# Kernel tuning notes

Hardware: AMD Instinct MI355X
Metric: run time of the kernel (lower is better)

Reference implementation:

```python
import jax, jax.numpy as jnp
import numpy as np

NODES_PER_GRAPH = 128


def _leaky(x):
    return jnp.where(x >= 0, x, 0.01 * x)


def _graph_conv(x, W, src, dst, w_e, n_nodes):
    # DGL GraphConv, norm='both', bias=False, with edge_weight.
    # Structural (unweighted) degrees, clamped to 1, as in DGL.
    ones = jnp.ones(src.shape[0], dtype=x.dtype)
    deg_out = jnp.clip(jax.ops.segment_sum(ones, src, num_segments=n_nodes), 1.0)
    deg_in = jnp.clip(jax.ops.segment_sum(ones, dst, num_segments=n_nodes), 1.0)
    x = x * (deg_out ** -0.5)[:, None]
    if W.shape[0] > W.shape[1]:  # in_feats > out_feats: project first (DGL order)
        x = x @ W
    msg = x[src] * w_e[:, None]                     # [E, d]
    agg = jax.ops.segment_sum(msg, dst, num_segments=n_nodes)
    agg = agg * (deg_in ** -0.5)[:, None]
    if W.shape[0] <= W.shape[1]:
        agg = agg @ W
    return agg


def setup_inputs() -> dict:
    key = jax.random.key(0)
    ks = jax.random.split(key, 8)
    N, E = 131072, 1048576
    in_feats, hidden, readout = 64, 256, 128
    return {
        "node_feats": jax.random.normal(ks[0], (N, in_feats), dtype=jnp.float32),
        "edge_weight": jax.random.uniform(ks[1], (E,), dtype=jnp.float32),
        "W1": jax.random.normal(ks[2], (in_feats, hidden), dtype=jnp.float32) * 0.1,
        "W2": jax.random.normal(ks[3], (hidden, readout), dtype=jnp.float32) * 0.05,
        "W_lin": jax.random.normal(ks[4], (readout, 64), dtype=jnp.float32) * 0.1,
        "W_cls": jax.random.normal(ks[5], (64, 16), dtype=jnp.float32) * 0.1,
        "edge_src": jax.random.randint(ks[6], (E,), 0, N, dtype=jnp.int32),
        "edge_dst": jax.random.randint(ks[7], (E,), 0, N, dtype=jnp.int32),
    }


def reference(node_feats, edge_weight, W1, W2, W_lin, W_cls, edge_src, edge_dst):
    N = node_feats.shape[0]
    G = N // NODES_PER_GRAPH
    h = _leaky(_graph_conv(node_feats, W1, edge_src, edge_dst, edge_weight, N))
    h = _leaky(_graph_conv(h, W2, edge_src, edge_dst, edge_weight, N))
    # mean_nodes readout over batched graphs of equal size
    gid = jnp.arange(N, dtype=jnp.int32) // NODES_PER_GRAPH
    pooled = jax.ops.segment_sum(h, gid, num_segments=G) / NODES_PER_GRAPH
    # linear -> dropout(eval: identity) -> classifier (no activation in head)
    return (pooled @ W_lin) @ W_cls
```

## Files before the change

### kernel.cpp

```cpp
#include <hip/hip_runtime.h>


constexpr int NPG = 128;
constexpr int F0  = 64;
constexpr int F1  = 256;
constexpr int F2  = 128;
constexpr int BMM = 64;
constexpr int H2  = 136;
constexpr int CAP = 40;
constexpr int NXCD = 8;

using bf16x8 = __attribute__((ext_vector_type(8))) short;
using f32x4  = __attribute__((ext_vector_type(4))) float;

__device__ __forceinline__ float leaky(float x) {
    return (x >= 0.f) ? x : 0.01f * x;
}

__device__ __forceinline__ unsigned short f2bf(float x) {
    unsigned u = __float_as_uint(x);
    return (unsigned short)((u + 0x7FFFu + ((u >> 16) & 1u)) >> 16);
}
__device__ __forceinline__ float bf2f(unsigned short h) {
    return __uint_as_float(((unsigned)h) << 16);
}
__device__ __forceinline__ void split2(float x, unsigned short& hi, unsigned short& lo) {
    hi = f2bf(x);
    lo = f2bf(x - bf2f(hi));
}

__device__ __forceinline__ f32x4 mfma16(bf16x8 a, bf16x8 b, f32x4 c) {
    return __builtin_amdgcn_mfma_f32_16x16x32_bf16(a, b, c, 0, 0, 0);
}


__global__ void k_count_fill(const int* __restrict__ src, const int* __restrict__ dst,
                             const float* __restrict__ we,
                             int* __restrict__ cnt_priv,
                             int* __restrict__ cnt_dst,
                             int2* __restrict__ slots, unsigned E, int N) {
    unsigned xcc;
    asm("s_getreg_b32 %0, hwreg(HW_REG_XCC_ID)" : "=s"(xcc));
    xcc &= (NXCD - 1);
    unsigned e = blockIdx.x * 256u + threadIdx.x;
    if (e < E) {
        const int s = src[e], d = dst[e];
        const int pos = atomicAdd(&cnt_dst[d], 1);
        if (pos < CAP) slots[(size_t)d * CAP + pos] = make_int2(s, __float_as_int(we[e]));
        __hip_atomic_fetch_add(&cnt_priv[(size_t)xcc * N + s], 1,
                               __ATOMIC_RELAXED, __HIP_MEMORY_SCOPE_WORKGROUP);
    }
}

__global__ void k_finalize_deg(const int* __restrict__ cnt_priv,
                               const int* __restrict__ cnt_dst,
                               float* __restrict__ dinv_out, float* __restrict__ dinv_in,
                               int N) {
    int i = blockIdx.x * blockDim.x + threadIdx.x;
    if (i < N) {
        int c = 0;
#pragma unroll
        for (int x = 0; x < NXCD; ++x) c += cnt_priv[(size_t)x * N + i];
        dinv_out[i] = rsqrtf((float)max(c, 1));
        dinv_in[i]  = rsqrtf((float)max(cnt_dst[i], 1));
    }
}

__global__ void __launch_bounds__(256) k_scale_w(
        int2* __restrict__ slots, const int* __restrict__ cnt_dst,
        const float* __restrict__ dinv_out, int N) {
    int gid = blockIdx.x * 256 + threadIdx.x;
    int n = gid >> 3;
    int j0 = gid & 7;
    if (n >= N) return;
    const int cnt = min(cnt_dst[n], CAP);
    for (int j = j0; j < cnt; j += 8) {
        const size_t idx = (size_t)n * CAP + j;
        int2 p = slots[idx];
        p.y = __float_as_int(__int_as_float(p.y) * dinv_out[p.x]);
        slots[idx] = p;
    }
}

__global__ void k_wsplit1(const float* __restrict__ W1,
                          unsigned short* __restrict__ w1h, unsigned short* __restrict__ w1l) {
    int i = blockIdx.x * 256 + threadIdx.x;
    if (i < F1 * F0) {
        int n = i >> 6, k = i & 63;
        unsigned short h, l;
        split2(W1[k * F1 + n], h, l);
        w1h[i] = h; w1l[i] = l;
    }
}
__global__ void k_wsplit2(const float* __restrict__ W2,
                          unsigned short* __restrict__ w2h, unsigned short* __restrict__ w2l) {
    int i = blockIdx.x * 256 + threadIdx.x;
    if (i < F2 * F1) {
        int n = i >> 8, k = i & 255;
        unsigned short h, l;
        split2(W2[k * F2 + n], h, l);
        w2h[i] = h; w2l[i] = l;
    }
}

__global__ void __launch_bounds__(256) k_gather1(
        const float4* __restrict__ featsv, const int* __restrict__ cnt_dst,
        const int2* __restrict__ slots, const float* __restrict__ dinv_in,
        unsigned short* __restrict__ a1h, unsigned short* __restrict__ a1l, int N) {
    const int gid = blockIdx.x * 256 + threadIdx.x;
    const int n = gid >> 4;
    const int s = gid & 15;
    if (n >= N) return;
    const size_t b = (size_t)n * CAP;
    const int cnt = min(cnt_dst[n], CAP);
    float4 acc = make_float4(0.f, 0.f, 0.f, 0.f);
    int j = 0;
    for (; j + 4 <= cnt; j += 4) {
        const int2 p0 = slots[b + j], p1 = slots[b + j + 1];
        const int2 p2 = slots[b + j + 2], p3 = slots[b + j + 3];
        const float4 v0 = featsv[(size_t)p0.x * 16 + s];
        const float4 v1 = featsv[(size_t)p1.x * 16 + s];
        const float4 v2 = featsv[(size_t)p2.x * 16 + s];
        const float4 v3 = featsv[(size_t)p3.x * 16 + s];
        const float w0 = __int_as_float(p0.y), w1 = __int_as_float(p1.y);
        const float w2 = __int_as_float(p2.y), w3 = __int_as_float(p3.y);
        acc.x = fmaf(v0.x, w0, acc.x); acc.y = fmaf(v0.y, w0, acc.y);
        acc.z = fmaf(v0.z, w0, acc.z); acc.w = fmaf(v0.w, w0, acc.w);
        acc.x = fmaf(v1.x, w1, acc.x); acc.y = fmaf(v1.y, w1, acc.y);
        acc.z = fmaf(v1.z, w1, acc.z); acc.w = fmaf(v1.w, w1, acc.w);
        acc.x = fmaf(v2.x, w2, acc.x); acc.y = fmaf(v2.y, w2, acc.y);
        acc.z = fmaf(v2.z, w2, acc.z); acc.w = fmaf(v2.w, w2, acc.w);
        acc.x = fmaf(v3.x, w3, acc.x); acc.y = fmaf(v3.y, w3, acc.y);
        acc.z = fmaf(v3.z, w3, acc.z); acc.w = fmaf(v3.w, w3, acc.w);
    }
    for (; j < cnt; ++j) {
        const int2 p = slots[b + j];
        const float4 v = featsv[(size_t)p.x * 16 + s];
        const float w = __int_as_float(p.y);
        acc.x = fmaf(v.x, w, acc.x); acc.y = fmaf(v.y, w, acc.y);
        acc.z = fmaf(v.z, w, acc.z); acc.w = fmaf(v.w, w, acc.w);
    }
    const float din = dinv_in[n];
    ushort4 h4, l4;
    split2(acc.x * din, h4.x, l4.x);
    split2(acc.y * din, h4.y, l4.y);
    split2(acc.z * din, h4.z, l4.z);
    split2(acc.w * din, h4.w, l4.w);
    const size_t off = (size_t)n * 64 + s * 4;
    *(ushort4*)(a1h + off) = h4;
    *(ushort4*)(a1l + off) = l4;
}

__global__ void __launch_bounds__(256, 4) k_mfma_fused(
        const unsigned short* __restrict__ a1h, const unsigned short* __restrict__ a1l,
        const unsigned short* __restrict__ w1h, const unsigned short* __restrict__ w1l,
        const unsigned short* __restrict__ w2h, const unsigned short* __restrict__ w2l,
        unsigned short* __restrict__ x2b) {
    __shared__ unsigned short hhi[BMM][H2];
    __shared__ unsigned short hlo[BMM][H2];
    const int tid  = threadIdx.x;
    const int w    = tid >> 6;
    const int lane = tid & 63;
    const int r    = lane & 15;
    const int kg   = lane >> 4;
    const int base = blockIdx.x * BMM;

    f32x4 acc1[4][4] = {};
#pragma unroll
    for (int ks = 0; ks < 2; ++ks) {
        const int kk = ks * 32 + kg * 8;
        bf16x8 wh[4], wl[4];
#pragma unroll
        for (int j = 0; j < 4; ++j) {
            const int col = (j >> 1) * 128 + w * 32 + (j & 1) * 16 + r;
            wh[j] = *(const bf16x8*)(w1h + col * F0 + kk);
            wl[j] = *(const bf16x8*)(w1l + col * F0 + kk);
        }
#pragma unroll
        for (int mt = 0; mt < 4; ++mt) {
            const size_t aoff = (size_t)(base + mt * 16 + r) * F0 + kk;
            const bf16x8 ah = *(const bf16x8*)(a1h + aoff);
            const bf16x8 al = *(const bf16x8*)(a1l + aoff);
#pragma unroll
            for (int j = 0; j < 4; ++j) {
                acc1[mt][j] = mfma16(ah, wh[j], acc1[mt][j]);
                acc1[mt][j] = mfma16(ah, wl[j], acc1[mt][j]);
                acc1[mt][j] = mfma16(al, wh[j], acc1[mt][j]);
            }
        }
    }

    f32x4 acc2[4][2] = {};
    const int c2base = w * 32;
#pragma unroll
    for (int h = 0; h < 2; ++h) {
#pragma unroll
        for (int jn = 0; jn < 2; ++jn) {
            const int j = h * 2 + jn;
            const int lc = w * 32 + jn * 16 + r;
#pragma unroll
            for (int mt = 0; mt < 4; ++mt)
#pragma unroll
                for (int i = 0; i < 4; ++i) {
                    const int rl = mt * 16 + kg * 4 + i;
                    unsigned short hi_, lo_;
                    split2(leaky(acc1[mt][j][i]), hi_, lo_);
                    hhi[rl][lc] = hi_;
                    hlo[rl][lc] = lo_;
                }
        }
        __syncthreads();
#pragma unroll
        for (int ks = 0; ks < 4; ++ks) {
            const int lkk = ks * 32 + kg * 8;
            const int kglob = h * 128 + lkk;
            bf16x8 w2hv[2], w2lv[2];
#pragma unroll
            for (int nt = 0; nt < 2; ++nt) {
                const int col = c2base + nt * 16 + r;
                w2hv[nt] = *(const bf16x8*)(w2h + col * F1 + kglob);
                w2lv[nt] = *(const bf16x8*)(w2l + col * F1 + kglob);
            }
#pragma unroll
            for (int mt = 0; mt < 4; ++mt) {
                const int rl = mt * 16 + r;
                const bf16x8 ah = *(const bf16x8*)&hhi[rl][lkk];
                const bf16x8 al = *(const bf16x8*)&hlo[rl][lkk];
#pragma unroll
                for (int nt = 0; nt < 2; ++nt) {
                    acc2[mt][nt] = mfma16(ah, w2hv[nt], acc2[mt][nt]);
                    acc2[mt][nt] = mfma16(ah, w2lv[nt], acc2[mt][nt]);
                    acc2[mt][nt] = mfma16(al, w2hv[nt], acc2[mt][nt]);
                }
            }
        }
        __syncthreads();
    }

#pragma unroll
    for (int mt = 0; mt < 4; ++mt)
#pragma unroll
        for (int nt = 0; nt < 2; ++nt)
#pragma unroll
            for (int i = 0; i < 4; ++i) {
                const int row = base + mt * 16 + kg * 4 + i;
                const int col = c2base + nt * 16 + r;
                x2b[(size_t)row * F2 + col] = f2bf(acc2[mt][nt][i]);
            }
}

__global__ void __launch_bounds__(256) k_gather2_pool4(
        const ushort4* __restrict__ x2v, const int* __restrict__ cnt_dst,
        const int2* __restrict__ slots, const float* __restrict__ dinv_in,
        float* __restrict__ pooled) {
    const int g = blockIdx.x >> 2;
    const int c = blockIdx.x & 3;
    const int t = threadIdx.x;
    const int q = t >> 3;
    const int s = t & 7;
    const int d4 = c * 8 + s;

    float4 pool = make_float4(0.f, 0.f, 0.f, 0.f);
    const int nbase = g * NPG;
#pragma unroll
    for (int i = 0; i < NPG; i += 32) {
        const int n = nbase + i + q;
        const size_t b = (size_t)n * CAP;
        const int cnt = min(cnt_dst[n], CAP);
        float4 acc = make_float4(0.f, 0.f, 0.f, 0.f);
        int j = 0;
        for (; j + 4 <= cnt; j += 4) {
            const int2 p0 = slots[b + j], p1 = slots[b + j + 1];
            const int2 p2 = slots[b + j + 2], p3 = slots[b + j + 3];
            const ushort4 u0 = x2v[(size_t)p0.x * 32 + d4];
            const ushort4 u1 = x2v[(size_t)p1.x * 32 + d4];
            const ushort4 u2 = x2v[(size_t)p2.x * 32 + d4];
            const ushort4 u3 = x2v[(size_t)p3.x * 32 + d4];
            const float w0 = __int_as_float(p0.y), w1 = __int_as_float(p1.y);
            const float w2 = __int_as_float(p2.y), w3 = __int_as_float(p3.y);
            acc.x = fmaf(bf2f(u0.x), w0, acc.x); acc.y = fmaf(bf2f(u0.y), w0, acc.y);
            acc.z = fmaf(bf2f(u0.z), w0, acc.z); acc.w = fmaf(bf2f(u0.w), w0, acc.w);
            acc.x = fmaf(bf2f(u1.x), w1, acc.x); acc.y = fmaf(bf2f(u1.y), w1, acc.y);
            acc.z = fmaf(bf2f(u1.z), w1, acc.z); acc.w = fmaf(bf2f(u1.w), w1, acc.w);
            acc.x = fmaf(bf2f(u2.x), w2, acc.x); acc.y = fmaf(bf2f(u2.y), w2, acc.y);
            acc.z = fmaf(bf2f(u2.z), w2, acc.z); acc.w = fmaf(bf2f(u2.w), w2, acc.w);
            acc.x = fmaf(bf2f(u3.x), w3, acc.x); acc.y = fmaf(bf2f(u3.y), w3, acc.y);
            acc.z = fmaf(bf2f(u3.z), w3, acc.z); acc.w = fmaf(bf2f(u3.w), w3, acc.w);
        }
        for (; j < cnt; ++j) {
            const int2 p = slots[b + j];
            const float w = __int_as_float(p.y);
            const ushort4 u = x2v[(size_t)p.x * 32 + d4];
            acc.x = fmaf(bf2f(u.x), w, acc.x); acc.y = fmaf(bf2f(u.y), w, acc.y);
            acc.z = fmaf(bf2f(u.z), w, acc.z); acc.w = fmaf(bf2f(u.w), w, acc.w);
        }
        const float din = dinv_in[n];
        pool.x += leaky(acc.x * din);
        pool.y += leaky(acc.y * din);
        pool.z += leaky(acc.z * din);
        pool.w += leaky(acc.w * din);
    }

    __shared__ float4 pl[32][8];
    pl[q][s] = pool;
    __syncthreads();
#pragma unroll
    for (int off = 16; off >= 1; off >>= 1) {
        if (q < off) {
            const float4 o = pl[q + off][s];
            pool.x += o.x; pool.y += o.y; pool.z += o.z; pool.w += o.w;
            pl[q][s] = pool;
        }
        __syncthreads();
    }
    if (q == 0) {
        const float inv = 1.0f / NPG;
        float4 r;
        r.x = pool.x * inv; r.y = pool.y * inv;
        r.z = pool.z * inv; r.w = pool.w * inv;
        ((float4*)pooled)[(size_t)g * 32 + d4] = r;
    }
}

__global__ void __launch_bounds__(64) k_head(
        const float* __restrict__ pooled,
        const float* __restrict__ Wlin,
        const float* __restrict__ Wcls,
        float* __restrict__ out) {
    const int g = blockIdx.x;
    const int t = threadIdx.x;
    __shared__ float p[F2];
    __shared__ float tj[64];
    p[t]      = pooled[(size_t)g * F2 + t];
    p[t + 64] = pooled[(size_t)g * F2 + 64 + t];
    __syncthreads();
    float s = 0.f;
#pragma unroll
    for (int k = 0; k < F2; ++k) s = fmaf(p[k], Wlin[k * 64 + t], s);
    tj[t] = s;
    __syncthreads();
    if (t < 16) {
        float sum = 0.f;
#pragma unroll
        for (int j = 0; j < 64; ++j) sum = fmaf(tj[j], Wcls[j * 16 + t], sum);
        out[g * 16 + t] = sum;
    }
}

extern "C" void kernel_launch(void* const* d_in, const int* in_sizes, int n_in,
                              void* d_out, int out_size, void* d_ws, size_t ws_size,
                              hipStream_t stream) {
    const float* feats = (const float*)d_in[0];
    const float* we    = (const float*)d_in[1];
    const float* W1    = (const float*)d_in[2];
    const float* W2    = (const float*)d_in[3];
    const float* Wlin  = (const float*)d_in[4];
    const float* Wcls  = (const float*)d_in[5];
    const int*   src   = (const int*)d_in[6];
    const int*   dst   = (const int*)d_in[7];

    const int N = in_sizes[0] / F0;
    const unsigned E = (unsigned)in_sizes[1];
    const int G = N / NPG;

    float* out = (float*)d_out;

    int* ws_i = (int*)d_ws;
    size_t o = 0;
    auto align4 = [&]() { o = (o + 3) & ~(size_t)3; };
    int* cnt_dst = ws_i + o; o += N;
    int* cnt_priv = ws_i + o; o += (size_t)NXCD * N;
    float* dinv_out = (float*)(ws_i + o); o += N;
    float* dinv_in  = (float*)(ws_i + o); o += N;
    align4();
    int2* slots = (int2*)(ws_i + o); o += 2 * (size_t)N * CAP;
    unsigned short* a1h = (unsigned short*)(ws_i + o); o += (size_t)N * 32;
    unsigned short* a1l = (unsigned short*)(ws_i + o); o += (size_t)N * 32;
    unsigned short* x2b = (unsigned short*)(ws_i + o); o += (size_t)N * 64;
    unsigned short* w1h = (unsigned short*)(ws_i + o); o += (F1 * F0) / 2;
    unsigned short* w1l = (unsigned short*)(ws_i + o); o += (F1 * F0) / 2;
    unsigned short* w2h = (unsigned short*)(ws_i + o); o += (F2 * F1) / 2;
    unsigned short* w2l = (unsigned short*)(ws_i + o); o += (F2 * F1) / 2;
    align4();
    float* pooled = (float*)(ws_i + o); o += (size_t)G * F2;

    hipMemsetAsync(cnt_dst, 0, (size_t)(1 + NXCD) * N * sizeof(int), stream);

    k_count_fill<<<(E + 255) / 256, 256, 0, stream>>>(
        src, dst, we, cnt_priv, cnt_dst, slots, E, N);

    k_finalize_deg<<<(N + 255) / 256, 256, 0, stream>>>(
        cnt_priv, cnt_dst, dinv_out, dinv_in, N);

    k_scale_w<<<(N * 8 + 255) / 256, 256, 0, stream>>>(slots, cnt_dst, dinv_out, N);

    k_wsplit1<<<(F1 * F0 + 255) / 256, 256, 0, stream>>>(W1, w1h, w1l);
    k_wsplit2<<<(F2 * F1 + 255) / 256, 256, 0, stream>>>(W2, w2h, w2l);

    k_gather1<<<(N * 16 + 255) / 256, 256, 0, stream>>>(
        (const float4*)feats, cnt_dst, slots, dinv_in, a1h, a1l, N);

    k_mfma_fused<<<N / BMM, 256, 0, stream>>>(a1h, a1l, w1h, w1l, w2h, w2l, x2b);

    k_gather2_pool4<<<G * 4, 256, 0, stream>>>(
        (const ushort4*)x2b, cnt_dst, slots, dinv_in, pooled);
    k_head<<<G, 64, 0, stream>>>(pooled, Wlin, Wcls, out);
}
```

Before: 314.4 us.

## Replace global atomic slot fill with per-XCD counted two-pass CSR build

Edge bucketing now first counts source and destination degrees in per-XCD private arrays. A finalize kernel turns the per-XCD destination counts into prefix bases, and a second edge pass fills slots using XCD-local atomics. The source-degree normalization is folded into the fill, so the separate slot-scaling kernel is gone. This avoids contended device-scope atomics at the cost of reading the edge list twice and doubling the memset size.

```diff
diff --git a/kernel.cpp b/kernel.cpp
--- a/kernel.cpp
+++ b/kernel.cpp
@@ -33,52 +33,64 @@
     return __builtin_amdgcn_mfma_f32_16x16x32_bf16(a, b, c, 0, 0, 0);
 }
 
-
-__global__ void k_count_fill(const int* __restrict__ src, const int* __restrict__ dst,
-                             const float* __restrict__ we,
-                             int* __restrict__ cnt_priv,
-                             int* __restrict__ cnt_dst,
-                             int2* __restrict__ slots, unsigned E, int N) {
+__device__ __forceinline__ unsigned get_xcc() {
     unsigned xcc;
     asm("s_getreg_b32 %0, hwreg(HW_REG_XCC_ID)" : "=s"(xcc));
-    xcc &= (NXCD - 1);
+    return xcc & (NXCD - 1);
+}
+
+
+__global__ void k_count(const int* __restrict__ src, const int* __restrict__ dst,
+                        int* __restrict__ cnt_dpriv, int* __restrict__ cnt_spriv,
+                        unsigned E, int N) {
+    const unsigned xcc = get_xcc();
+    unsigned e = blockIdx.x * 256u + threadIdx.x;
+    if (e < E) {
+        __hip_atomic_fetch_add(&cnt_dpriv[(size_t)xcc * N + dst[e]], 1,
+                               __ATOMIC_RELAXED, __HIP_MEMORY_SCOPE_WORKGROUP);
+        __hip_atomic_fetch_add(&cnt_spriv[(size_t)xcc * N + src[e]], 1,
+                               __ATOMIC_RELAXED, __HIP_MEMORY_SCOPE_WORKGROUP);
+    }
+}
+
+__global__ void k_finalize_bases(int* __restrict__ cnt_dpriv,
+                                 const int* __restrict__ cnt_spriv,
+                                 int* __restrict__ cnt_dst,
+                                 float* __restrict__ dinv_out, float* __restrict__ dinv_in,
+                                 int N) {
+    int i = blockIdx.x * blockDim.x + threadIdx.x;
+    if (i < N) {
+        int cs = 0;
+#pragma unroll
+        for (int x = 0; x < NXCD; ++x) cs += cnt_spriv[(size_t)x * N + i];
+        dinv_out[i] = rsqrtf((float)max(cs, 1));
+        int run = 0;
+#pragma unroll
+        for (int x = 0; x < NXCD; ++x) {
+            const size_t idx = (size_t)x * N + i;
+            const int c = cnt_dpriv[idx];
+            cnt_dpriv[idx] = run;
+            run += c;
+        }
+        cnt_dst[i] = run;
+        dinv_in[i] = rsqrtf((float)max(run, 1));
+    }
+}
+
+__global__ void k_fill(const int* __restrict__ src, const int* __restrict__ dst,
+                       const float* __restrict__ we, const float* __restrict__ dinv_out,
+                       int* __restrict__ cnt_dpriv, int2* __restrict__ slots,
+                       unsigned E, int N) {
+    const unsigned xcc = get_xcc();
     unsigned e = blockIdx.x * 256u + threadIdx.x;
     if (e < E) {
         const int s = src[e], d = dst[e];
-        const int pos = atomicAdd(&cnt_dst[d], 1);
-        if (pos < CAP) slots[(size_t)d * CAP + pos] = make_int2(s, __float_as_int(we[e]));
-        __hip_atomic_fetch_add(&cnt_priv[(size_t)xcc * N + s], 1,
-                               __ATOMIC_RELAXED, __HIP_MEMORY_SCOPE_WORKGROUP);
-    }
-}
-
-__global__ void k_finalize_deg(const int* __restrict__ cnt_priv,
-                               const int* __restrict__ cnt_dst,
-                               float* __restrict__ dinv_out, float* __restrict__ dinv_in,
-                               int N) {
-    int i = blockIdx.x * blockDim.x + threadIdx.x;
-    if (i < N) {
-        int c = 0;
-#pragma unroll
-        for (int x = 0; x < NXCD; ++x) c += cnt_priv[(size_t)x * N + i];
-        dinv_out[i] = rsqrtf((float)max(c, 1));
-        dinv_in[i]  = rsqrtf((float)max(cnt_dst[i], 1));
-    }
-}
-
-__global__ void __launch_bounds__(256) k_scale_w(
-        int2* __restrict__ slots, const int* __restrict__ cnt_dst,
-        const float* __restrict__ dinv_out, int N) {
-    int gid = blockIdx.x * 256 + threadIdx.x;
-    int n = gid >> 3;
-    int j0 = gid & 7;
-    if (n >= N) return;
-    const int cnt = min(cnt_dst[n], CAP);
-    for (int j = j0; j < cnt; j += 8) {
-        const size_t idx = (size_t)n * CAP + j;
-        int2 p = slots[idx];
-        p.y = __float_as_int(__int_as_float(p.y) * dinv_out[p.x]);
-        slots[idx] = p;
+        const int ret = __hip_atomic_fetch_add(&cnt_dpriv[(size_t)xcc * N + d], 1,
+                                               __ATOMIC_RELAXED, __HIP_MEMORY_SCOPE_WORKGROUP);
+        if (ret < CAP) {
+            const float wcomb = we[e] * dinv_out[s];
+            slots[(size_t)d * CAP + ret] = make_int2(s, __float_as_int(wcomb));
+        }
     }
 }
 
@@ -368,8 +380,9 @@
     int* ws_i = (int*)d_ws;
     size_t o = 0;
     auto align4 = [&]() { o = (o + 3) & ~(size_t)3; };
-    int* cnt_dst = ws_i + o; o += N;
-    int* cnt_priv = ws_i + o; o += (size_t)NXCD * N;
+    int* cnt_dst   = ws_i + o; o += N;
+    int* cnt_dpriv = ws_i + o; o += (size_t)NXCD * N;
+    int* cnt_spriv = ws_i + o; o += (size_t)NXCD * N;
     float* dinv_out = (float*)(ws_i + o); o += N;
     float* dinv_in  = (float*)(ws_i + o); o += N;
     align4();
@@ -384,15 +397,15 @@
     align4();
     float* pooled = (float*)(ws_i + o); o += (size_t)G * F2;
 
-    hipMemsetAsync(cnt_dst, 0, (size_t)(1 + NXCD) * N * sizeof(int), stream);
-
-    k_count_fill<<<(E + 255) / 256, 256, 0, stream>>>(
-        src, dst, we, cnt_priv, cnt_dst, slots, E, N);
-
-    k_finalize_deg<<<(N + 255) / 256, 256, 0, stream>>>(
-        cnt_priv, cnt_dst, dinv_out, dinv_in, N);
-
-    k_scale_w<<<(N * 8 + 255) / 256, 256, 0, stream>>>(slots, cnt_dst, dinv_out, N);
+    hipMemsetAsync(cnt_dpriv, 0, (size_t)2 * NXCD * N * sizeof(int), stream);
+
+    k_count<<<(E + 255) / 256, 256, 0, stream>>>(src, dst, cnt_dpriv, cnt_spriv, E, N);
+
+    k_finalize_bases<<<(N + 255) / 256, 256, 0, stream>>>(
+        cnt_dpriv, cnt_spriv, cnt_dst, dinv_out, dinv_in, N);
+
+    k_fill<<<(E + 255) / 256, 256, 0, stream>>>(
+        src, dst, we, dinv_out, cnt_dpriv, slots, E, N);
 
     k_wsplit1<<<(F1 * F0 + 255) / 256, 256, 0, stream>>>(W1, w1h, w1l);
     k_wsplit2<<<(F2 * F1 + 255) / 256, 256, 0, stream>>>(W2, w2h, w2l);
```

Result: slower. 360.3 us (+14.6%).
